# Kernel tuning notes

Measured on AMD Instinct MI355X. Metric: run time of the kernel, lower is better.

The kernel has to match this reference:

```python
import jax, jax.numpy as jnp
import numpy as np
from functools import partial

INPUT_DIM = 256
HIDDEN = 512
NUM_LAYERS = 2

def _linp(key, fan_in, shape):
    # torch nn.Linear/Conv default init: U(-1/sqrt(fan_in), 1/sqrt(fan_in))
    bound = 1.0 / np.sqrt(fan_in)
    return jax.random.uniform(key, shape, jnp.float32, -bound, bound)

def setup_inputs() -> dict:
    key = jax.random.key(0)
    ks = iter(jax.random.split(key, 64))
    d = {}
    d["x"] = jax.random.normal(next(ks), (32, 16, 1, 64, 64), jnp.float32)
    # encoder convs (OIHW)
    d["conv1_w"] = _linp(next(ks), 1 * 9, (16, 1, 3, 3));   d["conv1_b"] = _linp(next(ks), 1 * 9, (16,))
    d["conv2_w"] = _linp(next(ks), 16 * 9, (32, 16, 3, 3)); d["conv2_b"] = _linp(next(ks), 16 * 9, (32,))
    d["conv3_w"] = _linp(next(ks), 32 * 9, (INPUT_DIM, 32, 3, 3)); d["conv3_b"] = _linp(next(ks), 32 * 9, (INPUT_DIM,))
    # LSTM cells: per layer 4 gate linears (forget, input, cell, output), in = input+hidden
    for j in range(NUM_LAYERS):
        fan = (INPUT_DIM if j == 0 else HIDDEN) + HIDDEN
        for g in ("f", "i", "g", "o"):
            d[f"W{g}{j}"] = _linp(next(ks), fan, (fan, HIDDEN))
            d[f"b{g}{j}"] = _linp(next(ks), fan, (HIDDEN,))
    # classifier
    d["cw1"] = _linp(next(ks), HIDDEN, (HIDDEN, 128)); d["cb1"] = _linp(next(ks), HIDDEN, (128,))
    d["cw2"] = _linp(next(ks), 128, (128, 64));        d["cb2"] = _linp(next(ks), 128, (64,))
    d["cw3"] = _linp(next(ks), 64, (64, 6));           d["cb3"] = _linp(next(ks), 64, (6,))
    return d

def _conv(x, w, b):
    y = jax.lax.conv_general_dilated(x, w, (1, 1), "SAME",
                                     dimension_numbers=("NCHW", "OIHW", "NCHW"))
    return y + b[None, :, None, None]

def _maxpool2(x):
    return jax.lax.reduce_window(x, -jnp.inf, jax.lax.max,
                                 (1, 1, 2, 2), (1, 1, 2, 2), "VALID")

def reference(x, conv1_w, conv1_b, conv2_w, conv2_b, conv3_w, conv3_b,
              Wf0, bf0, Wi0, bi0, Wg0, bg0, Wo0, bo0,
              Wf1, bf1, Wi1, bi1, Wg1, bg1, Wo1, bo1,
              cw1, cb1, cw2, cb2, cw3, cb3):
    B, T, C, H, W = x.shape
    xf = x.reshape(B * T, C, H, W)
    h = _maxpool2(jax.nn.relu(_conv(xf, conv1_w, conv1_b)))
    h = _maxpool2(jax.nn.relu(_conv(h, conv2_w, conv2_b)))
    h = jax.nn.relu(_conv(h, conv3_w, conv3_b))
    emb = h.mean(axis=(2, 3)).reshape(B, T, -1)  # AdaptiveAvgPool2d((1,1)); dropout = identity (eval)

    layers = [(Wf0, bf0, Wi0, bi0, Wg0, bg0, Wo0, bo0),
              (Wf1, bf1, Wi1, bi1, Wg1, bg1, Wo1, bo1)]

    def step(carry, x_t):
        hs, cs = carry
        inp = x_t
        new_h, new_c = [], []
        for j, (Wf, bf, Wi, bi, Wg, bg, Wo, bo) in enumerate(layers):
            comb = jnp.concatenate([inp, hs[j]], axis=1)  # [B, in+H]
            f_t = jax.nn.sigmoid(comb @ Wf + bf)
            i_t = jax.nn.sigmoid(comb @ Wi + bi)
            g_t = jnp.tanh(comb @ Wg + bg)
            o_t = jax.nn.sigmoid(comb @ Wo + bo)
            c_n = f_t * cs[j] + i_t * g_t
            h_n = o_t * jnp.tanh(c_n)
            new_h.append(h_n); new_c.append(c_n)
            inp = h_n
        return (tuple(new_h), tuple(new_c)), None

    h0 = tuple(jnp.zeros((B, HIDDEN), x.dtype) for _ in range(NUM_LAYERS))
    c0 = tuple(jnp.zeros((B, HIDDEN), x.dtype) for _ in range(NUM_LAYERS))
    (hs, _), _ = jax.lax.scan(step, (h0, c0), jnp.swapaxes(emb, 0, 1))
    last = hs[-1]  # [B, HIDDEN], last timestep top-layer h (dropout = identity)

    y = jax.nn.relu(last @ cw1 + cb1)
    y = jax.nn.relu(y @ cw2 + cb2)
    return y @ cw3 + cb3  # [B, 6]
```

## Files before the change

### kernel.cpp

```cpp
#include <hip/hip_runtime.h>
#include <math.h>

__global__ void k_conv1(const float* __restrict__ x, const float* __restrict__ w,
                        const float* __restrict__ bias, float* __restrict__ out) {
  int idx = blockIdx.x * 256 + threadIdx.x;
  int ox = idx & 31, oy = (idx >> 5) & 31, oc = (idx >> 10) & 15, n = idx >> 14;
  const float* im = x + n * 4096;
  float wv[9];
#pragma unroll
  for (int i = 0; i < 9; ++i) wv[i] = w[oc * 9 + i];
  float bs = bias[oc];
  float m = 0.f;
#pragma unroll
  for (int dy = 0; dy < 2; ++dy)
#pragma unroll
    for (int dx = 0; dx < 2; ++dx) {
      int cy = oy * 2 + dy, cx = ox * 2 + dx;
      float s = bs;
#pragma unroll
      for (int ky = 0; ky < 3; ++ky) {
        int yy = cy + ky - 1;
        if (yy < 0 || yy >= 64) continue;
#pragma unroll
        for (int kx = 0; kx < 3; ++kx) {
          int xx = cx + kx - 1;
          if (xx < 0 || xx >= 64) continue;
          s += im[yy * 64 + xx] * wv[ky * 3 + kx];
        }
      }
      m = fmaxf(m, fmaxf(s, 0.f));
    }
  out[idx] = m;
}

__global__ void k_prep_w(const float* __restrict__ w2, float* __restrict__ w2t,
                         const float* __restrict__ w3, float* __restrict__ w3t) {
  int id = blockIdx.x * 256 + threadIdx.x;
  if (id < 73728) {
    int ct = id >> 8, oc = id & 255;
    int c = ct / 9, tap = ct - 9 * c;
    w3t[id] = w3[(oc * 32 + c) * 9 + tap];
  }
  if (id < 4608) {
    int ct = id >> 5, oc = id & 31;
    int c = ct / 9, tap = ct - 9 * c;
    w2t[id] = w2[(oc * 16 + c) * 9 + tap];
  }
}

__global__ __launch_bounds__(256) void k_conv2(
    const float* __restrict__ a1, const float* __restrict__ w2t,
    const float* __restrict__ bias, float* __restrict__ a2) {
  __shared__ __align__(16) float ins[8 * 1024];
  int n = blockIdx.x, ocg = blockIdx.y;
  int tid = threadIdx.x;
  int py = tid >> 4, px = tid & 15;
  int y0 = 2 * py - 1, x0 = 2 * px - 1;
  float acc[16][4] = {};
  const float* wb = w2t + ocg * 16;
  for (int ph = 0; ph < 2; ++ph) {
    __syncthreads();
    const float4* src = (const float4*)(a1 + n * 16384 + ph * 8192);
    for (int i = tid; i < 2048; i += 256) ((float4*)ins)[i] = src[i];
    __syncthreads();
    for (int c = 0; c < 8; ++c) {
      float wv[4][4];
#pragma unroll
      for (int r = 0; r < 4; ++r) {
        int y = y0 + r;
        bool vy = (y >= 0) && (y < 32);
        int yc = vy ? y : 0;
#pragma unroll
        for (int cc = 0; cc < 4; ++cc) {
          int xx = x0 + cc;
          bool vx = (xx >= 0) && (xx < 32);
          int xc = vx ? xx : 0;
          float t = ins[c * 1024 + yc * 32 + xc];
          wv[r][cc] = (vy && vx) ? t : 0.f;
        }
      }
      int ch = ph * 8 + c;
#pragma unroll
      for (int ky = 0; ky < 3; ++ky)
#pragma unroll
        for (int kx = 0; kx < 3; ++kx) {
          const float* w16 = wb + (ch * 9 + ky * 3 + kx) * 32;
#pragma unroll
          for (int i = 0; i < 4; ++i) {
            float vv = wv[(i >> 1) + ky][(i & 1) + kx];
#pragma unroll
            for (int j = 0; j < 16; ++j) acc[j][i] += vv * w16[j];
          }
        }
    }
  }
  const float* bp = bias + ocg * 16;
  float4 o[4];
#pragma unroll
  for (int j = 0; j < 16; ++j) {
    float m = fmaxf(fmaxf(acc[j][0], acc[j][1]), fmaxf(acc[j][2], acc[j][3]));
    ((float*)o)[j] = fmaxf(m + bp[j], 0.f);
  }
  float4* dst = (float4*)(a2 + (size_t)(n * 256 + tid) * 32 + ocg * 16);
#pragma unroll
  for (int q = 0; q < 4; ++q) dst[q] = o[q];
}

__global__ __launch_bounds__(512, 4) void k_conv3(
    const float* __restrict__ a2, const float* __restrict__ w3t,
    const float* __restrict__ bias, float* __restrict__ comb0) {
  __shared__ __align__(16) float ins[324 * 20];
  float4* ins4 = (float4*)ins;
  int n = blockIdx.x, ocb = blockIdx.y;
  int tid = threadIdx.x;
  for (int i = tid; i < 1620; i += 512) ins4[i] = float4{0.f, 0.f, 0.f, 0.f};
  int wvid = __builtin_amdgcn_readfirstlane(tid >> 6);
  int lane = tid & 63;
  int tr = lane >> 4, tc = lane & 15;
  float acc[4][16] = {};
  const float* wbase = w3t + ocb * 128 + wvid * 16;
  const float4* src = (const float4*)(a2 + (size_t)n * 8192);
  for (int hf = 0; hf < 2; ++hf) {
    __syncthreads();
    for (int i = tid; i < 1024; i += 512) {
      int px = i >> 2, cg = i & 3;
      int p = ((px >> 4) + 1) * 18 + (px & 15) + 1;
      ins4[p * 5 + cg] = src[px * 8 + hf * 4 + cg];
    }
    __syncthreads();
    for (int cg = 0; cg < 4; ++cg) {
      int chb = hf * 16 + cg * 4;
#pragma unroll
      for (int dr = 0; dr < 6; ++dr) {
#pragma unroll
        for (int dc = 0; dc < 3; ++dc) {
          int pp = (4 * tr + dr) * 18 + tc + dc;
          float4 v = ins4[pp * 5 + cg];
#pragma unroll
          for (int c = 0; c < 4; ++c) {
            float vv = ((const float*)&v)[c];
            const int ilo = (dr - 2 < 0) ? 0 : dr - 2;
            const int ihi = (dr < 3) ? dr : 3;
#pragma unroll
            for (int i = ilo; i <= ihi; ++i) {
              const float* w16 = wbase + (((chb + c) * 9 + (dr - i) * 3 + dc) * 256);
#pragma unroll
              for (int j = 0; j < 16; ++j) acc[i][j] += vv * w16[j];
            }
          }
        }
      }
    }
  }
  const float* bp = bias + ocb * 128 + wvid * 16;
  int bb = n >> 4, tt = n & 15;
#pragma unroll
  for (int j = 0; j < 16; ++j) {
    float bj = bp[j];
    float s = 0.f;
#pragma unroll
    for (int i = 0; i < 4; ++i) s += fmaxf(acc[i][j] + bj, 0.f);
#pragma unroll
    for (int off = 32; off; off >>= 1) s += __shfl_down(s, off, 64);
    if (lane == 0) {
      int oc = ocb * 128 + wvid * 16 + j;
      comb0[(size_t)(tt * 768 + oc) * 32 + bb] = s * (1.f / 256.f);
    }
  }
}

struct TPtrs { const float* in[8]; float* out[8]; };

__global__ void k_transpose(TPtrs p) {
  __shared__ float tile[32][33];
  int z = blockIdx.z;
  int fan = (z < 4) ? 768 : 1024;
  int k0 = blockIdx.x * 32, h0 = blockIdx.y * 32;
  if (k0 >= fan) return;
  const float* in = p.in[z];
  float* out = p.out[z];
  int tx = threadIdx.x, ty = threadIdx.y;
  for (int r = 0; r < 32; r += 8)
    tile[ty + r][tx] = in[(k0 + ty + r) * 512 + h0 + tx];
  __syncthreads();
  for (int r = 0; r < 32; r += 8)
    out[(h0 + ty + r) * fan + k0 + tx] = tile[tx][ty + r];
}

struct LstmArgs {
  const float* comb; float* houtA; float* houtB; float* cT;
  const float* Wf; const float* Wi; const float* Wg; const float* Wo;
  const float* bf; const float* bi; const float* bg; const float* bo;
};

template <int IN>
__device__ __forceinline__ void lstm_body(int h, int tid, const LstmArgs& A,
                                          float* wl, float* gsum, float* pre) {
  constexpr int FAN = IN + 512;
  constexpr int PR = FAN + 4;
  constexpr int KT = FAN / 16;
  if (tid < FAN / 4) {
    ((float4*)(wl + 0 * PR))[tid] = ((const float4*)(A.Wf + (size_t)h * FAN))[tid];
    ((float4*)(wl + 1 * PR))[tid] = ((const float4*)(A.Wi + (size_t)h * FAN))[tid];
    ((float4*)(wl + 2 * PR))[tid] = ((const float4*)(A.Wg + (size_t)h * FAN))[tid];
    ((float4*)(wl + 3 * PR))[tid] = ((const float4*)(A.Wo + (size_t)h * FAN))[tid];
  }
  __syncthreads();
  const int kq = (tid >> 3) & 15, c = tid >> 7, bq = tid & 7;
  const int kbase = kq * KT;
  const float4* w4 = (const float4*)(wl + c * PR + kbase);
  const float4* a4 = (const float4*)A.comb + bq;
  float acc0 = 0.f, acc1 = 0.f, acc2 = 0.f, acc3 = 0.f;
#pragma unroll
  for (int kk = 0; kk < KT / 4; ++kk) {
    float4 w = w4[kk];
#pragma unroll
    for (int j = 0; j < 4; ++j) {
      float wj = ((const float*)&w)[j];
      float4 a = a4[(size_t)(kbase + kk * 4 + j) * 8];
      acc0 += wj * a.x; acc1 += wj * a.y; acc2 += wj * a.z; acc3 += wj * a.w;
    }
  }
  ((float4*)(gsum + (c * 16 + kq) * 36))[bq] = float4{acc0, acc1, acc2, acc3};
  __syncthreads();
  if (tid < 128) {
    int cc = tid >> 5, b = tid & 31;
    float s = 0.f;
#pragma unroll
    for (int q = 0; q < 16; ++q) s += gsum[(cc * 16 + q) * 36 + b];
    pre[cc * 33 + b] = s;
  }
  __syncthreads();
  if (tid < 32) {
    int b = tid;
    float fp = pre[0 * 33 + b] + A.bf[h];
    float ip = pre[1 * 33 + b] + A.bi[h];
    float gp = pre[2 * 33 + b] + A.bg[h];
    float op = pre[3 * 33 + b] + A.bo[h];
    float ft = 1.f / (1.f + expf(-fp));
    float it = 1.f / (1.f + expf(-ip));
    float gt = tanhf(gp);
    float ot = 1.f / (1.f + expf(-op));
    float cn = ft * A.cT[h * 32 + b] + it * gt;
    A.cT[h * 32 + b] = cn;
    float hn = ot * tanhf(cn);
    A.houtA[h * 32 + b] = hn;
    A.houtB[h * 32 + b] = hn;
  }
}

template <int IN>
__global__ __launch_bounds__(512) void k_lstm(LstmArgs a) {
  __shared__ __align__(16) float wl[4 * 1028];
  __shared__ __align__(16) float gsum[4 * 16 * 36];
  __shared__ float pre[4 * 33];
  lstm_body<IN>(blockIdx.x, threadIdx.x, a, wl, gsum, pre);
}

__global__ __launch_bounds__(512) void k_lstm_pair(LstmArgs a0, LstmArgs a1) {
  __shared__ __align__(16) float wl[4 * 1028];
  __shared__ __align__(16) float gsum[4 * 16 * 36];
  __shared__ float pre[4 * 33];
  if (blockIdx.x < 512)
    lstm_body<256>(blockIdx.x, threadIdx.x, a0, wl, gsum, pre);
  else
    lstm_body<512>(blockIdx.x - 512, threadIdx.x, a1, wl, gsum, pre);
}

__global__ void k_cls(const float* __restrict__ h1T, const float* __restrict__ cw1,
                      const float* __restrict__ cb1, const float* __restrict__ cw2,
                      const float* __restrict__ cb2, const float* __restrict__ cw3,
                      const float* __restrict__ cb3, float* __restrict__ out) {
  __shared__ float hv[512];
  __shared__ float y1[128];
  __shared__ float y2[64];
  int b = blockIdx.x, tid = threadIdx.x;
  for (int i = tid; i < 512; i += 128) hv[i] = h1T[i * 32 + b];
  __syncthreads();
  float s = cb1[tid];
  for (int k = 0; k < 512; ++k) s += hv[k] * cw1[k * 128 + tid];
  y1[tid] = fmaxf(s, 0.f);
  __syncthreads();
  if (tid < 64) {
    float s2 = cb2[tid];
    for (int k = 0; k < 128; ++k) s2 += y1[k] * cw2[k * 64 + tid];
    y2[tid] = fmaxf(s2, 0.f);
  }
  __syncthreads();
  if (tid < 6) {
    float s3 = cb3[tid];
    for (int k = 0; k < 64; ++k) s3 += y2[k] * cw3[k * 6 + tid];
    out[b * 6 + tid] = s3;
  }
}

extern "C" void kernel_launch(void* const* d_in, const int* in_sizes, int n_in,
                              void* d_out, int out_size, void* d_ws, size_t ws_size,
                              hipStream_t stream) {
  const float* x  = (const float*)d_in[0];
  const float* w1 = (const float*)d_in[1];
  const float* b1 = (const float*)d_in[2];
  const float* w2 = (const float*)d_in[3];
  const float* b2 = (const float*)d_in[4];
  const float* w3 = (const float*)d_in[5];
  const float* b3 = (const float*)d_in[6];
  const float* cw1 = (const float*)d_in[23];
  const float* cb1 = (const float*)d_in[24];
  const float* cw2 = (const float*)d_in[25];
  const float* cb2 = (const float*)d_in[26];
  const float* cw3 = (const float*)d_in[27];
  const float* cb3 = (const float*)d_in[28];

  float* ws = (float*)d_ws;
  float* a1    = ws;
  float* wt    = ws;
  float* comb0 = ws + 3670016;
  float* comb1 = ws + 4087808;
  float* c0    = ws + 4644864;
  float* c1    = ws + 4661248;
  float* a2    = ws + 8388608;
  float* w2t   = ws + 12582912;
  float* w3t   = ws + 12587520;
  const int C0 = 768 * 32, C1 = 1024 * 32;

  k_prep_w<<<288, 256, 0, stream>>>(w2, w2t, w3, w3t);
  k_conv1<<<32768, 256, 0, stream>>>(x, w1, b1, a1);
  k_conv2<<<dim3(512, 2), 256, 0, stream>>>(a1, w2t, b2, a2);

  hipMemsetAsync(comb0 + 256 * 32, 0, (size_t)512 * 32 * 4, stream);
  hipMemsetAsync(comb1 + 512 * 32, 0, (size_t)512 * 32 * 4, stream);
  hipMemsetAsync(c0, 0, (size_t)2 * 512 * 32 * 4, stream);

  k_conv3<<<dim3(512, 2), 512, 0, stream>>>(a2, w3t, b3, comb0);

  TPtrs tp;
  for (int g = 0; g < 4; ++g) {
    tp.in[g]      = (const float*)d_in[7 + 2 * g];
    tp.out[g]     = wt + g * (512 * 768);
    tp.in[4 + g]  = (const float*)d_in[15 + 2 * g];
    tp.out[4 + g] = wt + 4 * (512 * 768) + g * (512 * 1024);
  }
  k_transpose<<<dim3(32, 16, 8), dim3(32, 8), 0, stream>>>(tp);

  const float* wl0[4] = {wt, wt + 393216, wt + 786432, wt + 1179648};
  float* l1base = wt + 1572864;
  const float* wl1[4] = {l1base, l1base + 524288, l1base + 1048576, l1base + 1572864};

  auto L0 = [&](int t) {
    LstmArgs a;
    a.comb = comb0 + (size_t)t * C0;
    a.houtA = comb0 + (size_t)(t + 1) * C0 + 256 * 32;
    a.houtB = comb1 + (size_t)t * C1;
    a.cT = c0;
    a.Wf = wl0[0]; a.Wi = wl0[1]; a.Wg = wl0[2]; a.Wo = wl0[3];
    a.bf = (const float*)d_in[8];  a.bi = (const float*)d_in[10];
    a.bg = (const float*)d_in[12]; a.bo = (const float*)d_in[14];
    return a;
  };
  auto L1 = [&](int t) {
    LstmArgs a;
    a.comb = comb1 + (size_t)t * C1;
    a.houtA = comb1 + (size_t)(t + 1) * C1 + 512 * 32;
    a.houtB = a.houtA;
    a.cT = c1;
    a.Wf = wl1[0]; a.Wi = wl1[1]; a.Wg = wl1[2]; a.Wo = wl1[3];
    a.bf = (const float*)d_in[16]; a.bi = (const float*)d_in[18];
    a.bg = (const float*)d_in[20]; a.bo = (const float*)d_in[22];
    return a;
  };

  k_lstm<256><<<512, 512, 0, stream>>>(L0(0));
  for (int p = 0; p < 15; ++p)
    k_lstm_pair<<<1024, 512, 0, stream>>>(L0(p + 1), L1(p));
  k_lstm<512><<<512, 512, 0, stream>>>(L1(15));

  k_cls<<<32, 128, 0, stream>>>(comb1 + (size_t)16 * C1 + 512 * 32,
                                cw1, cb1, cw2, cb2, cw3, cb3, (float*)d_out);
}
```

Baseline: 687.6 us.

## Run LSTM recurrence as one persistent cooperative kernel with grid sync

Replaces the 17 per-timestep LSTM kernel launches with one cooperative persistent kernel. Each of 256 blocks keeps its slice of gate weights for both layers (two hidden units each) resident in LDS and keeps the cell state in registers. Timesteps are separated by grid.sync, which removes launch overhead and repeated weight reloads from global memory each step. It relies on all 256 blocks being co-resident. If the cooperative launch fails, it falls back to the old multi-launch path. The conv3 inner loop is also restructured around the kernel-row index.

Measured after the change: 2.061 ms. +199.8%, slower.

```diff
diff --git a/kernel.cpp b/kernel.cpp
--- a/kernel.cpp
+++ b/kernel.cpp
@@ -1,5 +1,8 @@
 #include <hip/hip_runtime.h>
+#include <hip/hip_cooperative_groups.h>
 #include <math.h>
+
+namespace cg = cooperative_groups;
 
 __global__ void k_conv1(const float* __restrict__ x, const float* __restrict__ w,
                         const float* __restrict__ bias, float* __restrict__ out) {
@@ -139,13 +142,14 @@
 #pragma unroll
           for (int c = 0; c < 4; ++c) {
             float vv = ((const float*)&v)[c];
-            const int ilo = (dr - 2 < 0) ? 0 : dr - 2;
-            const int ihi = (dr < 3) ? dr : 3;
-#pragma unroll
-            for (int i = ilo; i <= ihi; ++i) {
-              const float* w16 = wbase + (((chb + c) * 9 + (dr - i) * 3 + dc) * 256);
-#pragma unroll
-              for (int j = 0; j < 16; ++j) acc[i][j] += vv * w16[j];
+#pragma unroll
+            for (int ky = 0; ky < 3; ++ky) {
+              int i = dr - ky;
+              if (i >= 0 && i < 4) {
+                const float* w16 = wbase + (((chb + c) * 9 + ky * 3 + dc) * 256);
+#pragma unroll
+                for (int j = 0; j < 16; ++j) acc[i][j] += vv * w16[j];
+              }
             }
           }
         }
@@ -187,6 +191,129 @@
     out[(h0 + ty + r) * fan + k0 + tx] = tile[tx][ty + r];
 }
 
+struct CoopArgs {
+  float* comb0; float* comb1;
+  const float* w00; const float* w01; const float* w02; const float* w03;
+  const float* w10; const float* w11; const float* w12; const float* w13;
+  const float* b00; const float* b01; const float* b02; const float* b03;
+  const float* b10; const float* b11; const float* b12; const float* b13;
+};
+
+#define COOP_LDS_BYTES (19208 * 4)
+
+template <int IN>
+__device__ __forceinline__ void lstm_step2(
+    int hbase, int tid, const float* __restrict__ comb,
+    const float* __restrict__ wl,
+    float* __restrict__ houtA, float* __restrict__ houtB,
+    const float* __restrict__ Bf, const float* __restrict__ Bi,
+    const float* __restrict__ Bg, const float* __restrict__ Bo,
+    float& creg, float* __restrict__ gsum, float* __restrict__ pre) {
+  constexpr int FAN = IN + 512;
+  constexpr int KT = FAN / 16;
+  constexpr int QN = KT / 4;
+  __syncthreads();
+  const int hs = tid >> 8;
+  const int c = (tid >> 6) & 3;
+  const int kq = (tid >> 2) & 15;
+  const int bq = tid & 3;
+  const int kbase = kq * KT;
+  const float4* w4 = (const float4*)(wl + (size_t)(hs * 4 + c) * FAN + kbase);
+  const float4* a4 = (const float4*)comb;
+  const int r = kq % QN;
+  float acc0 = 0.f, acc1 = 0.f, acc2 = 0.f, acc3 = 0.f;
+  float acc4 = 0.f, acc5 = 0.f, acc6 = 0.f, acc7 = 0.f;
+#pragma unroll
+  for (int kk = 0; kk < QN; ++kk) {
+    int idx = kk + r;
+    if (idx >= QN) idx -= QN;
+    float4 w = w4[idx];
+#pragma unroll
+    for (int j = 0; j < 4; ++j) {
+      float wj = ((const float*)&w)[j];
+      int k8 = (kbase + idx * 4 + j) * 8;
+      float4 a0 = a4[k8 + bq];
+      float4 a1 = a4[k8 + 4 + bq];
+      acc0 += wj * a0.x; acc1 += wj * a0.y; acc2 += wj * a0.z; acc3 += wj * a0.w;
+      acc4 += wj * a1.x; acc5 += wj * a1.y; acc6 += wj * a1.z; acc7 += wj * a1.w;
+    }
+  }
+  float4* grow = (float4*)(gsum + (size_t)((hs * 4 + c) * 16 + kq) * 36);
+  grow[bq] = float4{acc0, acc1, acc2, acc3};
+  grow[4 + bq] = float4{acc4, acc5, acc6, acc7};
+  __syncthreads();
+  if (tid < 256) {
+    int g = tid >> 5, b = tid & 31;
+    float s = 0.f;
+#pragma unroll
+    for (int q = 0; q < 16; ++q) s += gsum[(size_t)(g * 16 + q) * 36 + b];
+    pre[g * 33 + b] = s;
+  }
+  __syncthreads();
+  if (tid < 64) {
+    int hs2 = tid >> 5, b = tid & 31;
+    int hh = hbase + hs2;
+    float fp = pre[(hs2 * 4 + 0) * 33 + b] + Bf[hh];
+    float ip = pre[(hs2 * 4 + 1) * 33 + b] + Bi[hh];
+    float gp = pre[(hs2 * 4 + 2) * 33 + b] + Bg[hh];
+    float op = pre[(hs2 * 4 + 3) * 33 + b] + Bo[hh];
+    float ft = 1.f / (1.f + expf(-fp));
+    float it_ = 1.f / (1.f + expf(-ip));
+    float gt = tanhf(gp);
+    float ot = 1.f / (1.f + expf(-op));
+    float cn = ft * creg + it_ * gt;
+    creg = cn;
+    float hn = ot * tanhf(cn);
+    houtA[hh * 32 + b] = hn;
+    houtB[hh * 32 + b] = hn;
+  }
+}
+
+__global__ __launch_bounds__(512) void k_lstm_coop(CoopArgs A) {
+  extern __shared__ float smem[];
+  float* wl0 = smem;
+  float* wl1 = smem + 6144;
+  float* gsum = smem + 14336;
+  float* pre = smem + 18944;
+  const int tid = threadIdx.x;
+  const int hbase = blockIdx.x * 2;
+  {
+    const float* s0[4] = {A.w00, A.w01, A.w02, A.w03};
+    const float* s1[4] = {A.w10, A.w11, A.w12, A.w13};
+    for (int i = tid; i < 1536; i += 512) {
+      int hs = i / 768, rem = i - hs * 768;
+      int g = rem / 192, q = rem - g * 192;
+      ((float4*)(wl0 + (size_t)(hs * 4 + g) * 768))[q] =
+          ((const float4*)(s0[g] + (size_t)(hbase + hs) * 768))[q];
+    }
+    for (int i = tid; i < 2048; i += 512) {
+      int hs = i >> 10, rem = i & 1023;
+      int g = rem >> 8, q = rem & 255;
+      ((float4*)(wl1 + (size_t)(hs * 4 + g) * 1024))[q] =
+          ((const float4*)(s1[g] + (size_t)(hbase + hs) * 1024))[q];
+    }
+  }
+  float c0reg = 0.f, c1reg = 0.f;
+  const int C0 = 768 * 32, C1 = 1024 * 32;
+  cg::grid_group grid = cg::this_grid();
+  for (int it = 0; it <= 16; ++it) {
+    if (it < 16)
+      lstm_step2<256>(hbase, tid, A.comb0 + (size_t)it * C0, wl0,
+                      A.comb0 + (size_t)(it + 1) * C0 + 256 * 32,
+                      A.comb1 + (size_t)it * C1,
+                      A.b00, A.b01, A.b02, A.b03, c0reg, gsum, pre);
+    if (it >= 1)
+      lstm_step2<512>(hbase, tid, A.comb1 + (size_t)(it - 1) * C1, wl1,
+                      A.comb1 + (size_t)it * C1 + 512 * 32,
+                      A.comb1 + (size_t)it * C1 + 512 * 32,
+                      A.b10, A.b11, A.b12, A.b13, c1reg, gsum, pre);
+    if (it < 16) {
+      __threadfence();
+      grid.sync();
+    }
+  }
+}
+
 struct LstmArgs {
   const float* comb; float* houtA; float* houtB; float* cT;
   const float* Wf; const float* Wi; const float* Wg; const float* Wo;
@@ -233,15 +360,15 @@
   __syncthreads();
   if (tid < 32) {
     int b = tid;
-    float fp = pre[0 * 33 + b] + A.bf[h];
-    float ip = pre[1 * 33 + b] + A.bi[h];
-    float gp = pre[2 * 33 + b] + A.bg[h];
-    float op = pre[3 * 33 + b] + A.bo[h];
+    float fp = pre[b] + A.bf[h];
+    float ip = pre[33 + b] + A.bi[h];
+    float gp = pre[66 + b] + A.bg[h];
+    float op = pre[99 + b] + A.bo[h];
     float ft = 1.f / (1.f + expf(-fp));
-    float it = 1.f / (1.f + expf(-ip));
+    float it_ = 1.f / (1.f + expf(-ip));
     float gt = tanhf(gp);
     float ot = 1.f / (1.f + expf(-op));
-    float cn = ft * A.cT[h * 32 + b] + it * gt;
+    float cn = ft * A.cT[h * 32 + b] + it_ * gt;
     A.cT[h * 32 + b] = cn;
     float hn = ot * tanhf(cn);
     A.houtA[h * 32 + b] = hn;
@@ -317,7 +444,6 @@
   float* comb0 = ws + 3670016;
   float* comb1 = ws + 4087808;
   float* c0    = ws + 4644864;
-  float* c1    = ws + 4661248;
   float* a2    = ws + 8388608;
   float* w2t   = ws + 12582912;
   float* w3t   = ws + 12587520;
@@ -342,37 +468,51 @@
   }
   k_transpose<<<dim3(32, 16, 8), dim3(32, 8), 0, stream>>>(tp);
 
+  float* l1base = wt + 1572864;
   const float* wl0[4] = {wt, wt + 393216, wt + 786432, wt + 1179648};
-  float* l1base = wt + 1572864;
-  const float* wl1[4] = {l1base, l1base + 524288, l1base + 1048576, l1base + 1572864};
-
-  auto L0 = [&](int t) {
-    LstmArgs a;
-    a.comb = comb0 + (size_t)t * C0;
-    a.houtA = comb0 + (size_t)(t + 1) * C0 + 256 * 32;
-    a.houtB = comb1 + (size_t)t * C1;
-    a.cT = c0;
-    a.Wf = wl0[0]; a.Wi = wl0[1]; a.Wg = wl0[2]; a.Wo = wl0[3];
-    a.bf = (const float*)d_in[8];  a.bi = (const float*)d_in[10];
-    a.bg = (const float*)d_in[12]; a.bo = (const float*)d_in[14];
-    return a;
-  };
-  auto L1 = [&](int t) {
-    LstmArgs a;
-    a.comb = comb1 + (size_t)t * C1;
-    a.houtA = comb1 + (size_t)(t + 1) * C1 + 512 * 32;
-    a.houtB = a.houtA;
-    a.cT = c1;
-    a.Wf = wl1[0]; a.Wi = wl1[1]; a.Wg = wl1[2]; a.Wo = wl1[3];
-    a.bf = (const float*)d_in[16]; a.bi = (const float*)d_in[18];
-    a.bg = (const float*)d_in[20]; a.bo = (const float*)d_in[22];
-    return a;
-  };
-
-  k_lstm<256><<<512, 512, 0, stream>>>(L0(0));
-  for (int p = 0; p < 15; ++p)
-    k_lstm_pair<<<1024, 512, 0, stream>>>(L0(p + 1), L1(p));
-  k_lstm<512><<<512, 512, 0, stream>>>(L1(15));
+  const float* wl1[4] = {l1base, l1base + 524288, l1base + 1048576,
+                         l1base + 1572864};
+
+  CoopArgs ca;
+  ca.comb0 = comb0; ca.comb1 = comb1;
+  ca.w00 = wl0[0]; ca.w01 = wl0[1]; ca.w02 = wl0[2]; ca.w03 = wl0[3];
+  ca.w10 = wl1[0]; ca.w11 = wl1[1]; ca.w12 = wl1[2]; ca.w13 = wl1[3];
+  ca.b00 = (const float*)d_in[8];  ca.b01 = (const float*)d_in[10];
+  ca.b02 = (const float*)d_in[12]; ca.b03 = (const float*)d_in[14];
+  ca.b10 = (const float*)d_in[16]; ca.b11 = (const float*)d_in[18];
+  ca.b12 = (const float*)d_in[20]; ca.b13 = (const float*)d_in[22];
+  void* kargs[] = {&ca};
+  hipError_t cerr = hipLaunchCooperativeKernel(
+      (void*)k_lstm_coop, dim3(256), dim3(512), kargs, COOP_LDS_BYTES, stream);
+
+  if (cerr != hipSuccess) {
+    auto L0 = [&](int t) {
+      LstmArgs a;
+      a.comb = comb0 + (size_t)t * C0;
+      a.houtA = comb0 + (size_t)(t + 1) * C0 + 256 * 32;
+      a.houtB = comb1 + (size_t)t * C1;
+      a.cT = c0;
+      a.Wf = wl0[0]; a.Wi = wl0[1]; a.Wg = wl0[2]; a.Wo = wl0[3];
+      a.bf = (const float*)d_in[8];  a.bi = (const float*)d_in[10];
+      a.bg = (const float*)d_in[12]; a.bo = (const float*)d_in[14];
+      return a;
+    };
+    auto L1 = [&](int t) {
+      LstmArgs a;
+      a.comb = comb1 + (size_t)t * C1;
+      a.houtA = comb1 + (size_t)(t + 1) * C1 + 512 * 32;
+      a.houtB = a.houtA;
+      a.cT = c0 + 16384;
+      a.Wf = wl1[0]; a.Wi = wl1[1]; a.Wg = wl1[2]; a.Wo = wl1[3];
+      a.bf = (const float*)d_in[16]; a.bi = (const float*)d_in[18];
+      a.bg = (const float*)d_in[20]; a.bo = (const float*)d_in[22];
+      return a;
+    };
+    k_lstm<256><<<512, 512, 0, stream>>>(L0(0));
+    for (int p = 0; p < 15; ++p)
+      k_lstm_pair<<<1024, 512, 0, stream>>>(L0(p + 1), L1(p));
+    k_lstm<512><<<512, 512, 0, stream>>>(L1(15));
+  }
 
   k_cls<<<32, 128, 0, stream>>>(comb1 + (size_t)16 * C1 + 512 * 32,
                                 cw1, cb1, cw2, cb2, cw3, cb3, (float*)d_out);
```
